# Performance work log

Hardware: AMD Instinct MI355X
Metric: run time of the kernel (lower is better)

Reference implementation:

```python
import jax, jax.numpy as jnp
import numpy as np

NUM_PRIMITIVES = 1024
DIM = 1024
TAU = 0.5  # temperature used by LivingCodebook.discretize default


def setup_inputs() -> dict:
    key = jax.random.key(0)
    k1, k2 = jax.random.split(key)
    logits = jax.random.normal(k1, (8, 4096, NUM_PRIMITIVES), dtype=jnp.float32)
    # learned codebook (nn.Parameter torch.randn(K, D) * 0.02)
    primitives = jax.random.normal(k2, (NUM_PRIMITIVES, DIM), dtype=jnp.float32) * 0.02
    return {"logits": logits, "primitives": primitives}


def _gumbel_softmax_hard(logits, key, tau):
    # F.gumbel_softmax(logits, tau, hard=True): straight-through one-hot
    g = jax.random.gumbel(key, logits.shape, dtype=logits.dtype)
    y_soft = jax.nn.softmax((logits + g) / tau, axis=-1)  # [b,s,k]
    idx = jnp.argmax(y_soft, axis=-1)                     # [b,s]
    y_hard = jax.nn.one_hot(idx, logits.shape[-1], dtype=logits.dtype)
    # hard forward value, soft gradient
    y = y_hard + y_soft - jax.lax.stop_gradient(y_soft)
    return y, idx


def reference(logits, primitives):
    """LivingCodebook.discretize: hard gumbel-softmax selection + codebook gather
    (expressed as one-hot GEMM for straight-through grads), plus the
    activation_count update vectorized as a scatter-add."""
    noise_key = jax.random.key(42)
    weights, indices = _gumbel_softmax_hard(logits, noise_key, TAU)
    # embeddings = weights @ primitives : [b,s,k] x [k,d] -> [b,s,d]
    embeddings = jnp.einsum("bsk,kd->bsd", weights, primitives)
    # activation_count[idx] += 1 for every selected index (vectorized)
    counts = jnp.zeros((primitives.shape[0],), dtype=jnp.int32).at[indices.reshape(-1)].add(1)
    return embeddings, indices, counts
```

## Files before the change

kernel.cpp:

```cpp
#include <hip/hip_runtime.h>
#include <stdint.h>

#define NROWS   32768
#define KDIM    1024
#define EMB_OFF 33554432
#define IDX_OFF 33554432
#define CNT_OFF 33587200

__device__ __forceinline__ uint32_t rotl32(uint32_t x, int r) {
    return (x << r) | (x >> (32 - r));
}

__device__ __forceinline__ uint32_t threefry_bits(uint32_t ctr) {
    const uint32_t ks0 = 0u;
    const uint32_t ks1 = 42u;
    const uint32_t ks2 = 0x1BD11BDAu ^ 0u ^ 42u;

    uint32_t x0 = 0u + ks0;
    uint32_t x1 = ctr + ks1;

    x0 += x1; x1 = rotl32(x1, 13); x1 ^= x0;
    x0 += x1; x1 = rotl32(x1, 15); x1 ^= x0;
    x0 += x1; x1 = rotl32(x1, 26); x1 ^= x0;
    x0 += x1; x1 = rotl32(x1,  6); x1 ^= x0;
    x0 += ks1; x1 += ks2 + 1u;
    x0 += x1; x1 = rotl32(x1, 17); x1 ^= x0;
    x0 += x1; x1 = rotl32(x1, 29); x1 ^= x0;
    x0 += x1; x1 = rotl32(x1, 16); x1 ^= x0;
    x0 += x1; x1 = rotl32(x1, 24); x1 ^= x0;
    x0 += ks2; x1 += ks0 + 2u;
    x0 += x1; x1 = rotl32(x1, 13); x1 ^= x0;
    x0 += x1; x1 = rotl32(x1, 15); x1 ^= x0;
    x0 += x1; x1 = rotl32(x1, 26); x1 ^= x0;
    x0 += x1; x1 = rotl32(x1,  6); x1 ^= x0;
    x0 += ks0; x1 += ks1 + 3u;
    x0 += x1; x1 = rotl32(x1, 17); x1 ^= x0;
    x0 += x1; x1 = rotl32(x1, 29); x1 ^= x0;
    x0 += x1; x1 = rotl32(x1, 16); x1 ^= x0;
    x0 += x1; x1 = rotl32(x1, 24); x1 ^= x0;
    x0 += ks1; x1 += ks2 + 4u;
    x0 += x1; x1 = rotl32(x1, 13); x1 ^= x0;
    x0 += x1; x1 = rotl32(x1, 15); x1 ^= x0;
    x0 += x1; x1 = rotl32(x1, 26); x1 ^= x0;
    x0 += x1; x1 = rotl32(x1,  6); x1 ^= x0;
    x0 += ks2; x1 += ks0 + 5u;

    return x0 ^ x1;
}

__device__ __forceinline__ float gumbel_from_bits(uint32_t bits) {
    float f = __uint_as_float((bits >> 9) | 0x3f800000u) - 1.0f;
    float u = fmaxf(f, 1.17549435e-38f);
    return -logf(-logf(u));
}

__global__ __launch_bounds__(256) void gumbel_argmax_gather(
    const float* __restrict__ logits,
    const float* __restrict__ prim,
    float* __restrict__ out,
    int* __restrict__ counts)
{
    const int row = blockIdx.x;
    const int tid = threadIdx.x;
    const uint32_t base = (uint32_t)row * (uint32_t)KDIM;

    float bv = -INFINITY;
    int   bk = 0;
    #pragma unroll
    for (int m = 0; m < 4; ++m) {
        const int k = tid + m * 256;
        const uint32_t ctr = base + (uint32_t)k;
        const float g = gumbel_from_bits(threefry_bits(ctr));
        const float z = logits[base + (uint32_t)k] + g;
        if (z > bv) { bv = z; bk = k; }
    }

    #pragma unroll
    for (int off = 32; off > 0; off >>= 1) {
        const float ov = __shfl_down(bv, off);
        const int   ok = __shfl_down(bk, off);
        if (ov > bv || (ov == bv && ok < bk)) { bv = ov; bk = ok; }
    }

    __shared__ float s_v[4];
    __shared__ int   s_k[4];
    __shared__ int   s_idx;
    const int wave = tid >> 6;
    if ((tid & 63) == 0) { s_v[wave] = bv; s_k[wave] = bk; }
    __syncthreads();

    if (tid == 0) {
        float v = s_v[0]; int kk = s_k[0];
        #pragma unroll
        for (int w = 1; w < 4; ++w) {
            if (s_v[w] > v || (s_v[w] == v && s_k[w] < kk)) { v = s_v[w]; kk = s_k[w]; }
        }
        s_idx = kk;
        out[IDX_OFF + row] = (float)kk;
        atomicAdd(&counts[kk], 1);
    }
    __syncthreads();

    const int idx = s_idx;
    const float4* __restrict__ src = (const float4*)(prim + (size_t)idx * KDIM);
    float4* __restrict__ dst = (float4*)(out + (size_t)row * KDIM);
    dst[tid] = src[tid];
}

__global__ void counts_to_float(const int* __restrict__ counts, float* __restrict__ out) {
    const int t = blockIdx.x * blockDim.x + threadIdx.x;
    if (t < KDIM) out[t] = (float)counts[t];
}

extern "C" void kernel_launch(void* const* d_in, const int* in_sizes, int n_in,
                              void* d_out, int out_size, void* d_ws, size_t ws_size,
                              hipStream_t stream) {
    const float* logits = (const float*)d_in[0];
    const float* prim   = (const float*)d_in[1];
    float* out = (float*)d_out;
    int*   cnt = (int*)d_ws;

    hipMemsetAsync(d_ws, 0, KDIM * sizeof(int), stream);

    gumbel_argmax_gather<<<NROWS, 256, 0, stream>>>(logits, prim, out, cnt);
    counts_to_float<<<4, 256, 0, stream>>>(cnt, out + CNT_OFF);
}
```

Baseline: 252.6 us.

## Use fast log gumbel with top-2 tracking and precise tie-break fallback

Replaces the precise double logf in the Gumbel noise with hardware __logf plus a series expansion near u=1. Each row tracks its top-2 candidates, and the winner is recomputed with precise logf only when the margin is tiny, so the selected index should still match the exact result. Logits are now read as one contiguous float4 per thread instead of strided scalars. This trims transcendental cost, but it adds register pressure and extra shuffles in the reduction, and correctness depends on the chosen margin.

```diff
diff --git a/kernel.cpp b/kernel.cpp
--- a/kernel.cpp
+++ b/kernel.cpp
@@ -1,9 +1,9 @@
 #include <hip/hip_runtime.h>
 #include <stdint.h>
+#include <math.h>
 
 #define NROWS   32768
 #define KDIM    1024
-#define EMB_OFF 33554432
 #define IDX_OFF 33554432
 #define CNT_OFF 33587200
 
@@ -48,10 +48,38 @@
     return x0 ^ x1;
 }
 
-__device__ __forceinline__ float gumbel_from_bits(uint32_t bits) {
+__device__ __forceinline__ float fast_gumbel(uint32_t bits) {
     float f = __uint_as_float((bits >> 9) | 0x3f800000u) - 1.0f;
     float u = fmaxf(f, 1.17549435e-38f);
-    return -logf(-logf(u));
+    float s = 1.0f - u;
+    float p = fmaf(s, 0.14285714f, 0.16666667f);
+    p = fmaf(s, p, 0.2f);
+    p = fmaf(s, p, 0.25f);
+    p = fmaf(s, p, 0.33333333f);
+    p = fmaf(s, p, 0.5f);
+    float y_poly = fmaf(s * s, p, s);
+    float y_hw   = -__logf(u);
+    float y = (u >= 0.875f) ? y_poly : y_hw;
+    return -__logf(y);
+}
+
+__device__ float precise_z(const float* __restrict__ logits, uint32_t flat) {
+    uint32_t bits = threefry_bits(flat);
+    float f = __uint_as_float((bits >> 9) | 0x3f800000u) - 1.0f;
+    float u = fmaxf(f, 1.17549435e-38f);
+    float g = -logf(-logf(u));
+    return logits[flat] + g;
+}
+
+__device__ __forceinline__ void merge2(float& v1, int& k1, float& v2, int& k2,
+                                       float w1, int j1, float w2, int j2) {
+    bool bw = (w1 > v1) || (w1 == v1 && j1 < k1);
+    float t1 = bw ? w1 : v1;  int tk1 = bw ? j1 : k1;
+    float c  = bw ? v1 : w1;  int ck  = bw ? k1 : j1;
+    float d  = bw ? w2 : v2;  int dk  = bw ? j2 : k2;
+    bool cs = (c > d) || (c == d && ck < dk);
+    v1 = t1; k1 = tk1;
+    v2 = cs ? c : d;  k2 = cs ? ck : dk;
 }
 
 __global__ __launch_bounds__(256) void gumbel_argmax_gather(
@@ -64,36 +92,47 @@
     const int tid = threadIdx.x;
     const uint32_t base = (uint32_t)row * (uint32_t)KDIM;
 
-    float bv = -INFINITY;
-    int   bk = 0;
+    const float4 l4 = ((const float4*)(logits + base))[tid];
+    float v1 = -INFINITY, v2 = -INFINITY;
+    int   k1 = 0x7fffffff, k2 = 0x7fffffff;
+    const float lv[4] = {l4.x, l4.y, l4.z, l4.w};
     #pragma unroll
-    for (int m = 0; m < 4; ++m) {
-        const int k = tid + m * 256;
-        const uint32_t ctr = base + (uint32_t)k;
-        const float g = gumbel_from_bits(threefry_bits(ctr));
-        const float z = logits[base + (uint32_t)k] + g;
-        if (z > bv) { bv = z; bk = k; }
+    for (int j = 0; j < 4; ++j) {
+        const int k = tid * 4 + j;
+        const float g = fast_gumbel(threefry_bits(base + (uint32_t)k));
+        const float z = lv[j] + g;
+        if (z > v1)      { v2 = v1; k2 = k1; v1 = z; k1 = k; }
+        else if (z > v2) { v2 = z;  k2 = k; }
     }
 
     #pragma unroll
     for (int off = 32; off > 0; off >>= 1) {
-        const float ov = __shfl_down(bv, off);
-        const int   ok = __shfl_down(bk, off);
-        if (ov > bv || (ov == bv && ok < bk)) { bv = ov; bk = ok; }
+        const float w1 = __shfl_down(v1, off);
+        const int   j1 = __shfl_down(k1, off);
+        const float w2 = __shfl_down(v2, off);
+        const int   j2 = __shfl_down(k2, off);
+        merge2(v1, k1, v2, k2, w1, j1, w2, j2);
     }
 
-    __shared__ float s_v[4];
-    __shared__ int   s_k[4];
+    __shared__ float s_v1[4], s_v2[4];
+    __shared__ int   s_k1[4], s_k2[4];
     __shared__ int   s_idx;
     const int wave = tid >> 6;
-    if ((tid & 63) == 0) { s_v[wave] = bv; s_k[wave] = bk; }
+    if ((tid & 63) == 0) { s_v1[wave] = v1; s_k1[wave] = k1; s_v2[wave] = v2; s_k2[wave] = k2; }
     __syncthreads();
 
     if (tid == 0) {
-        float v = s_v[0]; int kk = s_k[0];
+        float a1 = s_v1[0], a2 = s_v2[0];
+        int   b1 = s_k1[0], b2 = s_k2[0];
         #pragma unroll
-        for (int w = 1; w < 4; ++w) {
-            if (s_v[w] > v || (s_v[w] == v && s_k[w] < kk)) { v = s_v[w]; kk = s_k[w]; }
+        for (int w = 1; w < 4; ++w)
+            merge2(a1, b1, a2, b2, s_v1[w], s_k1[w], s_v2[w], s_k2[w]);
+
+        int kk = b1;
+        if (a1 - a2 <= 1e-4f) {
+            const float z1 = precise_z(logits, base + (uint32_t)b1);
+            const float z2 = precise_z(logits, base + (uint32_t)b2);
+            if (z2 > z1 || (z2 == z1 && b2 < b1)) kk = b2;
         }
         s_idx = kk;
         out[IDX_OFF + row] = (float)kk;
```

Measured after the change: 261.7 us. 3.6% more time.

## Replace gumbel log-log with exp/rcp packed keys and exact fallback on near-ties

Applied to the files above, without the earlier changes.

Reformulates the argmax of logits+gumbel as the argmax of exp(l)/(-log u), using fast hardware exp, log and reciprocal plus a series for u near 1, and packs the truncated value and index into one uint32 key. A top-2 reduction flags rows whose best two keys are close, and only those rows recompute with the precise log-log path. It also uses alignbit for the rotates and vectorised float4 logit loads. This cuts transcendental and compare cost, at the price of a divergent fallback path and its extra syncs.

```diff
diff --git a/kernel.cpp b/kernel.cpp
--- a/kernel.cpp
+++ b/kernel.cpp
@@ -1,14 +1,14 @@
 #include <hip/hip_runtime.h>
 #include <stdint.h>
+#include <math.h>
 
 #define NROWS   32768
 #define KDIM    1024
-#define EMB_OFF 33554432
 #define IDX_OFF 33554432
 #define CNT_OFF 33587200
 
 __device__ __forceinline__ uint32_t rotl32(uint32_t x, int r) {
-    return (x << r) | (x >> (32 - r));
+    return __builtin_amdgcn_alignbit(x, x, (uint32_t)(32 - r));
 }
 
 __device__ __forceinline__ uint32_t threefry_bits(uint32_t ctr) {
@@ -48,10 +48,25 @@
     return x0 ^ x1;
 }
 
-__device__ __forceinline__ float gumbel_from_bits(uint32_t bits) {
+__device__ __forceinline__ uint32_t fast_key(uint32_t bits, float l, int k) {
     float f = __uint_as_float((bits >> 9) | 0x3f800000u) - 1.0f;
     float u = fmaxf(f, 1.17549435e-38f);
-    return -logf(-logf(u));
+    float e_hw = -__logf(u);
+    float s = 1.0f - u;
+    float t = fmaf(s, 0.25f, 0.33333333f);
+    t = fmaf(s, t, 0.5f);
+    t = fmaf(s, t, 1.0f);
+    float e = (u >= 0.9375f) ? (s * t) : e_hw;
+    float R = __expf(l) * __builtin_amdgcn_rcpf(e);
+    return (__float_as_uint(R) & 0xFFFFFC00u) | (uint32_t)(k ^ 1023);
+}
+
+__device__ float precise_z(const float* __restrict__ logits, uint32_t flat) {
+    uint32_t bits = threefry_bits(flat);
+    float f = __uint_as_float((bits >> 9) | 0x3f800000u) - 1.0f;
+    float u = fmaxf(f, 1.17549435e-38f);
+    float g = -logf(-logf(u));
+    return logits[flat] + g;
 }
 
 __global__ __launch_bounds__(256) void gumbel_argmax_gather(
@@ -64,44 +79,82 @@
     const int tid = threadIdx.x;
     const uint32_t base = (uint32_t)row * (uint32_t)KDIM;
 
-    float bv = -INFINITY;
-    int   bk = 0;
+    const float4 l4 = ((const float4*)(logits + base))[tid];
+    const float lv[4] = {l4.x, l4.y, l4.z, l4.w};
+    uint32_t top1 = 0u, top2 = 0u;
     #pragma unroll
-    for (int m = 0; m < 4; ++m) {
-        const int k = tid + m * 256;
-        const uint32_t ctr = base + (uint32_t)k;
-        const float g = gumbel_from_bits(threefry_bits(ctr));
-        const float z = logits[base + (uint32_t)k] + g;
-        if (z > bv) { bv = z; bk = k; }
+    for (int j = 0; j < 4; ++j) {
+        const int k = tid * 4 + j;
+        const uint32_t key = fast_key(threefry_bits(base + (uint32_t)k), lv[j], k);
+        const uint32_t mn = min(key, top1);
+        top1 = max(key, top1);
+        top2 = max(top2, mn);
     }
 
     #pragma unroll
     for (int off = 32; off > 0; off >>= 1) {
-        const float ov = __shfl_down(bv, off);
-        const int   ok = __shfl_down(bk, off);
-        if (ov > bv || (ov == bv && ok < bk)) { bv = ov; bk = ok; }
+        const uint32_t o1 = (uint32_t)__shfl_down((int)top1, off);
+        const uint32_t o2 = (uint32_t)__shfl_down((int)top2, off);
+        top2 = max(top2, max(o2, min(top1, o1)));
+        top1 = max(top1, o1);
     }
 
-    __shared__ float s_v[4];
-    __shared__ int   s_k[4];
-    __shared__ int   s_idx;
+    __shared__ uint32_t s_t1[4], s_t2[4];
+    __shared__ int s_idx;
+    __shared__ int s_flag;
     const int wave = tid >> 6;
-    if ((tid & 63) == 0) { s_v[wave] = bv; s_k[wave] = bk; }
+    if ((tid & 63) == 0) { s_t1[wave] = top1; s_t2[wave] = top2; }
     __syncthreads();
 
     if (tid == 0) {
-        float v = s_v[0]; int kk = s_k[0];
+        uint32_t t1 = s_t1[0], t2 = s_t2[0];
         #pragma unroll
         for (int w = 1; w < 4; ++w) {
-            if (s_v[w] > v || (s_v[w] == v && s_k[w] < kk)) { v = s_v[w]; kk = s_k[w]; }
+            const uint32_t o1 = s_t1[w], o2 = s_t2[w];
+            t2 = max(t2, max(o2, min(t1, o1)));
+            t1 = max(t1, o1);
         }
-        s_idx = kk;
-        out[IDX_OFF + row] = (float)kk;
-        atomicAdd(&counts[kk], 1);
+        const int flag = ((t1 >> 10) - (t2 >> 10)) <= 7u;
+        s_flag = flag;
+        if (!flag) s_idx = (int)((t1 & 1023u) ^ 1023u);
     }
     __syncthreads();
 
+    if (s_flag) {
+        float bv = -INFINITY;
+        int   bk = 0x7fffffff;
+        #pragma unroll
+        for (int j = 0; j < 4; ++j) {
+            const int k = tid * 4 + j;
+            const float z = precise_z(logits, base + (uint32_t)k);
+            if (z > bv) { bv = z; bk = k; }
+        }
+        #pragma unroll
+        for (int off = 32; off > 0; off >>= 1) {
+            const float ov = __shfl_down(bv, off);
+            const int   ok = __shfl_down(bk, off);
+            if (ov > bv || (ov == bv && ok < bk)) { bv = ov; bk = ok; }
+        }
+        __shared__ float s_v[4];
+        __shared__ int   s_k[4];
+        if ((tid & 63) == 0) { s_v[wave] = bv; s_k[wave] = bk; }
+        __syncthreads();
+        if (tid == 0) {
+            float v = s_v[0]; int kk = s_k[0];
+            #pragma unroll
+            for (int w = 1; w < 4; ++w)
+                if (s_v[w] > v || (s_v[w] == v && s_k[w] < kk)) { v = s_v[w]; kk = s_k[w]; }
+            s_idx = kk;
+        }
+        __syncthreads();
+    }
+
     const int idx = s_idx;
+    if (tid == 0) {
+        out[IDX_OFF + row] = (float)idx;
+        atomicAdd(&counts[idx], 1);
+    }
+
     const float4* __restrict__ src = (const float4*)(prim + (size_t)idx * KDIM);
     float4* __restrict__ dst = (float4*)(out + (size_t)row * KDIM);
     dst[tid] = src[tid];
```

After: 252.8 us. Within noise of the previous version (+0.1%).
